# Kernel tuning notes

Measured on AMD Instinct MI355X. Metric: run time of the kernel, lower is better.

## Reference

```python
import jax, jax.numpy as jnp
import numpy as np
from jax import lax

DN = ('NHWC', 'HWIO', 'NHWC')

def hard_sigmoid(x):
    # Keras ConvLSTM2D default recurrent_activation
    return jnp.clip(0.2 * x + 0.5, 0.0, 1.0)

def conv2d_same(x, w):
    return lax.conv_general_dilated(x, w, (1, 1), 'SAME', dimension_numbers=DN)

def convlstm_layer(x, Wx, Wh, b):
    # x: [B,T,H,W,Cin]; Wx: [kh,kw,Cin,4F]; Wh: [kh,kw,F,4F]; b: [4F]
    B, T, H, W, Cin = x.shape
    F = Wh.shape[2]
    # Precompute input-to-gate convs for all timesteps in one big conv (same math).
    xg = conv2d_same(x.reshape(B * T, H, W, Cin), Wx).reshape(B, T, H, W, 4 * F) + b
    xg = jnp.moveaxis(xg, 1, 0)  # [T,B,H,W,4F]
    h0 = jnp.zeros((B, H, W, F), x.dtype)
    c0 = jnp.zeros((B, H, W, F), x.dtype)

    def step(carry, xg_t):
        h, c = carry
        gates = xg_t + conv2d_same(h, Wh)
        i, f, g, o = jnp.split(gates, 4, axis=-1)
        i = hard_sigmoid(i)
        f = hard_sigmoid(f)
        g = jnp.tanh(g)
        o = hard_sigmoid(o)
        c = f * c + i * g
        h = o * jnp.tanh(c)
        return (h, c), h

    (h, c), hs = lax.scan(step, (h0, c0), xg)
    outputs = jnp.moveaxis(hs, 0, 1)  # [B,T,H,W,F]
    return outputs, h, c

def setup_inputs() -> dict:
    key = jax.random.key(0)
    ks = jax.random.split(key, 8)
    B, T, H, W, Cin = 8, 10, 64, 64, 1
    F = 64
    k = 3
    sc = lambda fan: 1.0 / np.sqrt(fan)
    x = jax.random.normal(ks[0], (B, T, H, W, Cin), jnp.float32)
    Wx0 = jax.random.normal(ks[1], (k, k, Cin, 4 * F), jnp.float32) * sc(k * k * Cin)
    Wh0 = jax.random.normal(ks[2], (k, k, F, 4 * F), jnp.float32) * sc(k * k * F)
    b0 = jax.random.normal(ks[3], (4 * F,), jnp.float32) * 0.01
    Wx1 = jax.random.normal(ks[4], (k, k, F, 4 * F), jnp.float32) * sc(k * k * F)
    Wh1 = jax.random.normal(ks[5], (k, k, F, 4 * F), jnp.float32) * sc(k * k * F)
    b1 = jax.random.normal(ks[6], (4 * F,), jnp.float32) * 0.01
    return {'x': x, 'Wx0': Wx0, 'Wh0': Wh0, 'b0': b0, 'Wx1': Wx1, 'Wh1': Wh1, 'b1': b1}

def reference(x, Wx0, Wh0, b0, Wx1, Wh1, b1):
    out0, h0, c0 = convlstm_layer(x, Wx0, Wh0, b0)
    out1, h1, c1 = convlstm_layer(out0, Wx1, Wh1, b1)
    # Encoder returns per-layer [hidden_state, cell_state]; stack: [L,2,B,H,W,F]
    return jnp.stack([jnp.stack([h0, c0]), jnp.stack([h1, c1])])
```

## Files before the change

### kernel.cpp

```cpp
#include <hip/hip_runtime.h>


typedef _Float16 f16x8 __attribute__((ext_vector_type(8)));
typedef float f32x4 __attribute__((ext_vector_type(4)));

#define BHWF (8 * 64 * 64 * 64)
#define TSTRIDE 72
#define NCELL 180

__device__ __forceinline__ float hsig(float x) {
    return fminf(fmaxf(fmaf(0.2f, x, 0.5f), 0.0f), 1.0f);
}

__device__ __forceinline__ float ftanh(float x) {
    float e = __expf(2.0f * x);
    return fmaf(-2.0f, __builtin_amdgcn_rcpf(e + 1.0f), 1.0f);
}

__device__ __forceinline__ ushort f2h(float f) {
    _Float16 h = (_Float16)f;
    return __builtin_bit_cast(ushort, h);
}

__global__ void prep_w(const float* __restrict__ s0, const float* __restrict__ s1,
                       const float* __restrict__ s2, const float* __restrict__ wx0,
                       ushort* __restrict__ d0, ushort* __restrict__ d1,
                       ushort* __restrict__ d2, ushort* __restrict__ dx0) {
    int o = blockIdx.x * 256 + threadIdx.x;
    if (blockIdx.y == 3) {
        if (o < 8192) {
            int e    = o & 7;
            int lane = (o >> 3) & 63;
            int g    = (o >> 9) & 3;
            int fq   = (o >> 11) & 3;
            int k = (lane >> 4) * 8 + e;
            int n = g * 64 + fq * 16 + (lane & 15);
            dx0[o] = (k < 9) ? f2h(wx0[k * 256 + n]) : (ushort)0;
        }
        return;
    }
    const float* s[3] = { s0, s1, s2 };
    ushort* d[3] = { d0, d1, d2 };
    int e    = o & 7;
    int lane = (o >> 3) & 63;
    int g    = (o >> 9) & 3;
    int fq   = (o >> 11) & 3;
    int kc   = (o >> 13) & 1;
    int tap  = o >> 14;
    int n = g * 64 + fq * 16 + (lane & 15);
    int k = tap * 64 + kc * 32 + (lane >> 4) * 8 + e;
    d[blockIdx.y][o] = f2h(s[blockIdx.y][k * 256 + n]);
}

__device__ __forceinline__ void stage(const ushort* __restrict__ src,
                                      ushort* __restrict__ tile,
                                      int y0, int x0, int tid) {
    for (int v = tid; v < NCELL * 8; v += 256) {
        int cell = v >> 3, j = v & 7;
        int r = cell / 18, cc = cell - r * 18;
        int y = y0 - 1 + r, xx = x0 - 1 + cc;
        uint4 dv = make_uint4(0u, 0u, 0u, 0u);
        if ((unsigned)y < 64u && (unsigned)xx < 64u)
            dv = ((const uint4*)src)[(size_t)((y << 6) + xx) * 8 + j];
        *(uint4*)&tile[cell * TSTRIDE + j * 8] = dv;
    }
}

__device__ __forceinline__ void dma4(const ushort* __restrict__ src, ushort* dst) {
#pragma unroll
    for (int g = 0; g < 4; ++g)
        __builtin_amdgcn_global_load_lds(
            (const __attribute__((address_space(1))) unsigned int*)(src + g * 512),
            (__attribute__((address_space(3))) unsigned int*)(dst + g * 512),
            16, 0, 0);
}

__device__ __forceinline__ void conv_stream(const ushort* __restrict__ tile,
                                            const ushort* __restrict__ WS,
                                            ushort* __restrict__ bbuf,
                                            f32x4 (&acc)[8][4],
                                            int fq, int lane) {
    const int colA = lane & 15;
    const int quad = (lane >> 4) & 3;
    const int sl = fq * 2048 + lane * 8;
    dma4(WS + sl, bbuf + sl);
    f16x8 A[10];
#pragma unroll
    for (int c = 0; c < 18; ++c) {
        if (c < 17) {
            const int c1 = c + 1;
            const int kc1 = c1 / 9, dx1 = (c1 % 9) / 3, dy1 = c1 % 3;
            dma4(WS + (size_t)((dy1 * 3 + dx1) * 2 + kc1) * 8192 + sl,
                 bbuf + (c1 & 1) * 8192 + sl);
            __asm__ volatile("s_waitcnt vmcnt(4)" ::: "memory");
        } else {
            __asm__ volatile("s_waitcnt vmcnt(0)" ::: "memory");
        }
        const int kc = c / 9, dx = (c % 9) / 3, dy = c % 3;
        if (dy == 0) {
#pragma unroll
            for (int r = 0; r < 10; ++r)
                A[r] = *(const f16x8*)&tile[(r * 18 + colA + dx) * TSTRIDE + kc * 32 + quad * 8];
        }
        const ushort* bp = bbuf + (c & 1) * 8192 + sl;
        f16x8 B0 = *(const f16x8*)&bp[0];
        f16x8 B1 = *(const f16x8*)&bp[512];
        f16x8 B2 = *(const f16x8*)&bp[1024];
        f16x8 B3 = *(const f16x8*)&bp[1536];
#pragma unroll
        for (int mt = 0; mt < 8; ++mt) {
            acc[mt][0] = __builtin_amdgcn_mfma_f32_16x16x32_f16(A[mt + dy], B0, acc[mt][0], 0, 0, 0);
            acc[mt][1] = __builtin_amdgcn_mfma_f32_16x16x32_f16(A[mt + dy], B1, acc[mt][1], 0, 0, 0);
            acc[mt][2] = __builtin_amdgcn_mfma_f32_16x16x32_f16(A[mt + dy], B2, acc[mt][2], 0, 0, 0);
            acc[mt][3] = __builtin_amdgcn_mfma_f32_16x16x32_f16(A[mt + dy], B3, acc[mt][3], 0, 0, 0);
        }
    }
}

__global__ __launch_bounds__(256, 2) void step_merged(
    int l0_active, int l1_active, int last0, int last1,
    const float* __restrict__ x, const ushort* __restrict__ Wx0F,
    const ushort* __restrict__ Wh0S, const float* __restrict__ b0,
    const ushort* __restrict__ h0_prev, float* __restrict__ c0,
    ushort* __restrict__ h0_out, float* __restrict__ oh0, float* __restrict__ oc0,
    const ushort* __restrict__ xin, const ushort* __restrict__ Wx1S,
    const ushort* __restrict__ Wh1S, const float* __restrict__ b1,
    const ushort* __restrict__ h1_prev, float* __restrict__ c1,
    ushort* __restrict__ h1_out, float* __restrict__ oh1, float* __restrict__ oc1)
{
    __shared__ __align__(16) ushort tile[NCELL * TSTRIDE];
    __shared__ __align__(16) ushort bbuf[2 * 8192];
    __shared__ __align__(16) ushort xa[4096];

    const int z = blockIdx.z;
    bool isL1; int b;
    if (l0_active && l1_active) { isL1 = (z >= 8); b = z & 7; }
    else                        { isL1 = (l1_active != 0); b = z; }

    const int tid = threadIdx.x;
    const int lane = tid & 63;
    const int fq = tid >> 6;
    const int colA = lane & 15;
    const int quad = (lane >> 4) & 3;
    const int x0 = blockIdx.x * 16, y0 = blockIdx.y * 8;
    const int f = fq * 16 + colA;

    const ushort* h_prev = isL1 ? h1_prev : h0_prev;
    const float*  bias   = isL1 ? b1 : b0;
    float*        cbuf   = isL1 ? c1 : c0;
    ushort*       hout   = isL1 ? h1_out : h0_out;
    float* hf = isL1 ? (last1 ? oh1 : nullptr) : (last0 ? oh0 : nullptr);
    float* cf = isL1 ? (last1 ? oc1 : nullptr) : (last0 ? oc0 : nullptr);

    if (!isL1) {
        const float* xs = x + (size_t)b * 40960;
        for (int idx = tid; idx < 4096; idx += 256) {
            int e = idx & 7, li = (idx >> 3) & 63, r = idx >> 9;
            int ci = li & 15, qi = li >> 4;
            int k = qi * 8 + e;
            ushort val = 0;
            if (k < 9) {
                int dy = (k * 86) >> 8;
                int dx = k - dy * 3;
                int y = y0 + r + dy - 1, xx = x0 + ci + dx - 1;
                if ((unsigned)y < 64u && (unsigned)xx < 64u)
                    val = f2h(xs[(y << 6) + xx]);
            }
            xa[idx] = val;
        }
        if (h_prev) stage(h_prev + (size_t)b * 4096 * 64, tile, y0, x0, tid);
    } else {
        stage(xin + (size_t)b * 4096 * 64, tile, y0, x0, tid);
    }
    __syncthreads();

    f32x4 acc[8][4];
#pragma unroll
    for (int g = 0; g < 4; ++g) {
        float bv = bias[g * 64 + f];
#pragma unroll
        for (int mt = 0; mt < 8; ++mt) {
            acc[mt][g][0] = bv; acc[mt][g][1] = bv;
            acc[mt][g][2] = bv; acc[mt][g][3] = bv;
        }
    }

    if (!isL1) {
        f16x8 xb[4];
#pragma unroll
        for (int g = 0; g < 4; ++g)
            xb[g] = *(const f16x8*)&Wx0F[((fq * 4 + g) * 64 + lane) * 8];
#pragma unroll
        for (int mt = 0; mt < 8; ++mt) {
            f16x8 xaf = *(const f16x8*)&xa[mt * 512 + lane * 8];
#pragma unroll
            for (int g = 0; g < 4; ++g)
                acc[mt][g] = __builtin_amdgcn_mfma_f32_16x16x32_f16(
                    xaf, xb[g], acc[mt][g], 0, 0, 0);
        }
        if (h_prev) conv_stream(tile, Wh0S, bbuf, acc, fq, lane);
    } else {
        conv_stream(tile, Wx1S, bbuf, acc, fq, lane);
        if (h_prev) {
            __syncthreads();
            stage(h_prev + (size_t)b * 4096 * 64, tile, y0, x0, tid);
            __syncthreads();
            conv_stream(tile, Wh1S, bbuf, acc, fq, lane);
        }
    }

#pragma unroll
    for (int mt = 0; mt < 8; ++mt) {
        const int y = y0 + mt;
#pragma unroll
        for (int reg = 0; reg < 4; ++reg) {
            const int xx = x0 + quad * 4 + reg;
            const size_t cidx = ((size_t)((((b * 4 + fq) * 64 + y) * 4 + reg) * 16
                                 + (x0 >> 2) + quad)) * 16 + colA;
            const size_t pidx = ((size_t)b * 4096 + (y << 6) + xx) * 64 + f;
            float cp = h_prev ? cbuf[cidx] : 0.f;
            float iv = hsig(acc[mt][0][reg]);
            float fv = hsig(acc[mt][1][reg]);
            float gv = ftanh(acc[mt][2][reg]);
            float ov = hsig(acc[mt][3][reg]);
            float cn = fmaf(fv, cp, iv * gv);
            float hn = ov * ftanh(cn);
            cbuf[cidx] = cn;
            hout[pidx] = f2h(hn);
            if (hf) { hf[pidx] = hn; cf[pidx] = cn; }
        }
    }
}

extern "C" void kernel_launch(void* const* d_in, const int* in_sizes, int n_in,
                              void* d_out, int out_size, void* d_ws, size_t ws_size,
                              hipStream_t stream) {
    const float* x   = (const float*)d_in[0];
    const float* Wx0 = (const float*)d_in[1];
    const float* Wh0 = (const float*)d_in[2];
    const float* b0  = (const float*)d_in[3];
    const float* Wx1 = (const float*)d_in[4];
    const float* Wh1 = (const float*)d_in[5];
    const float* b1  = (const float*)d_in[6];
    float* out = (float*)d_out;
    char* ws = (char*)d_ws;

    ushort* h0buf[2] = { (ushort*)ws, (ushort*)(ws + 4u * 1024 * 1024) };
    ushort* h1buf[2] = { (ushort*)(ws + 8u * 1024 * 1024), (ushort*)(ws + 12u * 1024 * 1024) };
    float* c0 = (float*)(ws + 16u * 1024 * 1024);
    float* c1 = (float*)(ws + 24u * 1024 * 1024);
    ushort* Wh0S = (ushort*)(ws + 32u * 1024 * 1024);
    ushort* Wx1S = Wh0S + 147456;
    ushort* Wh1S = Wx1S + 147456;
    ushort* Wx0F = Wh1S + 147456;

    prep_w<<<dim3(576, 4), 256, 0, stream>>>(Wh0, Wx1, Wh1, Wx0,
                                             Wh0S, Wx1S, Wh1S, Wx0F);

    for (int t = 0; t <= 10; ++t) {
        const int has0 = (t < 10), has1 = (t >= 1);
        const int s = t - 1;
        const int tx = has0 ? t : 9;
        dim3 grid(4, 8, (has0 && has1) ? 16 : 8);
        step_merged<<<grid, 256, 0, stream>>>(
            has0, has1, (t == 9), (s == 9),
            x + (size_t)tx * 4096, Wx0F,
            (t >= 1) ? Wh0S : nullptr, b0,
            (t >= 1 && has0) ? h0buf[(t - 1) & 1] : nullptr, c0,
            h0buf[t & 1], out, out + BHWF,
            has1 ? h0buf[s & 1] : nullptr, Wx1S,
            Wh1S, b1,
            (s >= 1) ? h1buf[(s - 1) & 1] : nullptr, c1,
            h1buf[s & 1], out + 2 * (size_t)BHWF, out + 3 * (size_t)BHWF);
    }
}
```

Before: 461.0 us.

## Halve spatial tile height, load weights to registers, raise occupancy to four blocks

```diff
diff --git a/kernel.cpp b/kernel.cpp
--- a/kernel.cpp
+++ b/kernel.cpp
@@ -6,7 +6,7 @@
 
 #define BHWF (8 * 64 * 64 * 64)
 #define TSTRIDE 72
-#define NCELL 180
+#define NCELL 108
 
 __device__ __forceinline__ float hsig(float x) {
     return fminf(fmaxf(fmaf(0.2f, x, 0.5f), 0.0f), 1.0f);
@@ -66,58 +66,44 @@
     }
 }
 
-__device__ __forceinline__ void dma4(const ushort* __restrict__ src, ushort* dst) {
-#pragma unroll
-    for (int g = 0; g < 4; ++g)
-        __builtin_amdgcn_global_load_lds(
-            (const __attribute__((address_space(1))) unsigned int*)(src + g * 512),
-            (__attribute__((address_space(3))) unsigned int*)(dst + g * 512),
-            16, 0, 0);
-}
-
 __device__ __forceinline__ void conv_stream(const ushort* __restrict__ tile,
                                             const ushort* __restrict__ WS,
-                                            ushort* __restrict__ bbuf,
-                                            f32x4 (&acc)[8][4],
+                                            f32x4 (&acc)[4][4],
                                             int fq, int lane) {
     const int colA = lane & 15;
     const int quad = (lane >> 4) & 3;
-    const int sl = fq * 2048 + lane * 8;
-    dma4(WS + sl, bbuf + sl);
-    f16x8 A[10];
+    const ushort* wbase = WS + fq * 2048 + lane * 8;
+    f16x8 B[2][4];
+#pragma unroll
+    for (int g = 0; g < 4; ++g)
+        B[0][g] = *(const f16x8*)&wbase[g * 512];
 #pragma unroll
     for (int c = 0; c < 18; ++c) {
         if (c < 17) {
             const int c1 = c + 1;
             const int kc1 = c1 / 9, dx1 = (c1 % 9) / 3, dy1 = c1 % 3;
-            dma4(WS + (size_t)((dy1 * 3 + dx1) * 2 + kc1) * 8192 + sl,
-                 bbuf + (c1 & 1) * 8192 + sl);
-            __asm__ volatile("s_waitcnt vmcnt(4)" ::: "memory");
-        } else {
-            __asm__ volatile("s_waitcnt vmcnt(0)" ::: "memory");
+            const int f1 = (dy1 * 3 + dx1) * 2 + kc1;
+#pragma unroll
+            for (int g = 0; g < 4; ++g)
+                B[c1 & 1][g] = *(const f16x8*)&wbase[(size_t)f1 * 8192 + g * 512];
         }
         const int kc = c / 9, dx = (c % 9) / 3, dy = c % 3;
-        if (dy == 0) {
-#pragma unroll
-            for (int r = 0; r < 10; ++r)
-                A[r] = *(const f16x8*)&tile[(r * 18 + colA + dx) * TSTRIDE + kc * 32 + quad * 8];
-        }
-        const ushort* bp = bbuf + (c & 1) * 8192 + sl;
-        f16x8 B0 = *(const f16x8*)&bp[0];
-        f16x8 B1 = *(const f16x8*)&bp[512];
-        f16x8 B2 = *(const f16x8*)&bp[1024];
-        f16x8 B3 = *(const f16x8*)&bp[1536];
-#pragma unroll
-        for (int mt = 0; mt < 8; ++mt) {
-            acc[mt][0] = __builtin_amdgcn_mfma_f32_16x16x32_f16(A[mt + dy], B0, acc[mt][0], 0, 0, 0);
-            acc[mt][1] = __builtin_amdgcn_mfma_f32_16x16x32_f16(A[mt + dy], B1, acc[mt][1], 0, 0, 0);
-            acc[mt][2] = __builtin_amdgcn_mfma_f32_16x16x32_f16(A[mt + dy], B2, acc[mt][2], 0, 0, 0);
-            acc[mt][3] = __builtin_amdgcn_mfma_f32_16x16x32_f16(A[mt + dy], B3, acc[mt][3], 0, 0, 0);
-        }
-    }
-}
-
-__global__ __launch_bounds__(256, 2) void step_merged(
+        const ushort* ap = &tile[(dy * 18 + colA + dx) * TSTRIDE + kc * 32 + quad * 8];
+        f16x8 a0 = *(const f16x8*)&ap[0 * 18 * TSTRIDE];
+        f16x8 a1 = *(const f16x8*)&ap[1 * 18 * TSTRIDE];
+        f16x8 a2 = *(const f16x8*)&ap[2 * 18 * TSTRIDE];
+        f16x8 a3 = *(const f16x8*)&ap[3 * 18 * TSTRIDE];
+#pragma unroll
+        for (int g = 0; g < 4; ++g) {
+            acc[0][g] = __builtin_amdgcn_mfma_f32_16x16x32_f16(a0, B[c & 1][g], acc[0][g], 0, 0, 0);
+            acc[1][g] = __builtin_amdgcn_mfma_f32_16x16x32_f16(a1, B[c & 1][g], acc[1][g], 0, 0, 0);
+            acc[2][g] = __builtin_amdgcn_mfma_f32_16x16x32_f16(a2, B[c & 1][g], acc[2][g], 0, 0, 0);
+            acc[3][g] = __builtin_amdgcn_mfma_f32_16x16x32_f16(a3, B[c & 1][g], acc[3][g], 0, 0, 0);
+        }
+    }
+}
+
+__global__ __launch_bounds__(256, 4) void step_merged(
     int l0_active, int l1_active, int last0, int last1,
     const float* __restrict__ x, const ushort* __restrict__ Wx0F,
     const ushort* __restrict__ Wh0S, const float* __restrict__ b0,
@@ -129,8 +115,7 @@
     ushort* __restrict__ h1_out, float* __restrict__ oh1, float* __restrict__ oc1)
 {
     __shared__ __align__(16) ushort tile[NCELL * TSTRIDE];
-    __shared__ __align__(16) ushort bbuf[2 * 8192];
-    __shared__ __align__(16) ushort xa[4096];
+    __shared__ __align__(16) ushort xa[2048];
 
     const int z = blockIdx.z;
     bool isL1; int b;
@@ -142,7 +127,7 @@
     const int fq = tid >> 6;
     const int colA = lane & 15;
     const int quad = (lane >> 4) & 3;
-    const int x0 = blockIdx.x * 16, y0 = blockIdx.y * 8;
+    const int x0 = blockIdx.x * 16, y0 = blockIdx.y * 4;
     const int f = fq * 16 + colA;
 
     const ushort* h_prev = isL1 ? h1_prev : h0_prev;
@@ -154,7 +139,7 @@
 
     if (!isL1) {
         const float* xs = x + (size_t)b * 40960;
-        for (int idx = tid; idx < 4096; idx += 256) {
+        for (int idx = tid; idx < 2048; idx += 256) {
             int e = idx & 7, li = (idx >> 3) & 63, r = idx >> 9;
             int ci = li & 15, qi = li >> 4;
             int k = qi * 8 + e;
@@ -174,12 +159,12 @@
     }
     __syncthreads();
 
-    f32x4 acc[8][4];
+    f32x4 acc[4][4];
 #pragma unroll
     for (int g = 0; g < 4; ++g) {
         float bv = bias[g * 64 + f];
 #pragma unroll
-        for (int mt = 0; mt < 8; ++mt) {
+        for (int mt = 0; mt < 4; ++mt) {
             acc[mt][g][0] = bv; acc[mt][g][1] = bv;
             acc[mt][g][2] = bv; acc[mt][g][3] = bv;
         }
@@ -191,26 +176,26 @@
         for (int g = 0; g < 4; ++g)
             xb[g] = *(const f16x8*)&Wx0F[((fq * 4 + g) * 64 + lane) * 8];
 #pragma unroll
-        for (int mt = 0; mt < 8; ++mt) {
+        for (int mt = 0; mt < 4; ++mt) {
             f16x8 xaf = *(const f16x8*)&xa[mt * 512 + lane * 8];
 #pragma unroll
             for (int g = 0; g < 4; ++g)
                 acc[mt][g] = __builtin_amdgcn_mfma_f32_16x16x32_f16(
                     xaf, xb[g], acc[mt][g], 0, 0, 0);
         }
-        if (h_prev) conv_stream(tile, Wh0S, bbuf, acc, fq, lane);
+        if (h_prev) conv_stream(tile, Wh0S, acc, fq, lane);
     } else {
-        conv_stream(tile, Wx1S, bbuf, acc, fq, lane);
+        conv_stream(tile, Wx1S, acc, fq, lane);
         if (h_prev) {
             __syncthreads();
             stage(h_prev + (size_t)b * 4096 * 64, tile, y0, x0, tid);
             __syncthreads();
-            conv_stream(tile, Wh1S, bbuf, acc, fq, lane);
-        }
-    }
-
-#pragma unroll
-    for (int mt = 0; mt < 8; ++mt) {
+            conv_stream(tile, Wh1S, acc, fq, lane);
+        }
+    }
+
+#pragma unroll
+    for (int mt = 0; mt < 4; ++mt) {
         const int y = y0 + mt;
 #pragma unroll
         for (int reg = 0; reg < 4; ++reg) {
@@ -261,7 +246,7 @@
         const int has0 = (t < 10), has1 = (t >= 1);
         const int s = t - 1;
         const int tx = has0 ? t : 9;
-        dim3 grid(4, 8, (has0 && has1) ? 16 : 8);
+        dim3 grid(4, 16, (has0 && has1) ? 16 : 8);
         step_merged<<<grid, 256, 0, stream>>>(
             has0, has1, (t == 9), (s == 9),
             x + (size_t)tx * 4096, Wx0F,
```

New measurement: 586.6 us. 1.27x slower.

## Share weight frames across block with triple-buffered cooperative DMA and barriers

Applied to the files above, without the earlier changes.

```diff
diff --git a/kernel.cpp b/kernel.cpp
--- a/kernel.cpp
+++ b/kernel.cpp
@@ -66,12 +66,18 @@
     }
 }
 
-__device__ __forceinline__ void dma4(const ushort* __restrict__ src, ushort* dst) {
-#pragma unroll
-    for (int g = 0; g < 4; ++g)
+__device__ __forceinline__ int frame_of(int c) {
+    int kc = c / 9, r = c % 9, dxx = r / 3, dyy = r % 3;
+    return (dyy * 3 + dxx) * 2 + kc;
+}
+
+__device__ __forceinline__ void dma_frame(const ushort* __restrict__ src,
+                                          ushort* __restrict__ dst, int tid) {
+#pragma unroll
+    for (int s = 0; s < 4; ++s)
         __builtin_amdgcn_global_load_lds(
-            (const __attribute__((address_space(1))) unsigned int*)(src + g * 512),
-            (__attribute__((address_space(3))) unsigned int*)(dst + g * 512),
+            (const __attribute__((address_space(1))) unsigned int*)(src + s * 2048 + tid * 8),
+            (__attribute__((address_space(3))) unsigned int*)(dst + s * 2048 + tid * 8),
             16, 0, 0);
 }
 
@@ -79,30 +85,27 @@
                                             const ushort* __restrict__ WS,
                                             ushort* __restrict__ bbuf,
                                             f32x4 (&acc)[8][4],
-                                            int fq, int lane) {
+                                            int fq, int lane, int tid) {
     const int colA = lane & 15;
     const int quad = (lane >> 4) & 3;
-    const int sl = fq * 2048 + lane * 8;
-    dma4(WS + sl, bbuf + sl);
+    __syncthreads();
+    dma_frame(WS + (size_t)frame_of(0) * 8192, bbuf, tid);
+    dma_frame(WS + (size_t)frame_of(1) * 8192, bbuf + 8192, tid);
+    __asm__ volatile("s_waitcnt vmcnt(4)\ns_barrier" ::: "memory");
     f16x8 A[10];
 #pragma unroll
     for (int c = 0; c < 18; ++c) {
-        if (c < 17) {
-            const int c1 = c + 1;
-            const int kc1 = c1 / 9, dx1 = (c1 % 9) / 3, dy1 = c1 % 3;
-            dma4(WS + (size_t)((dy1 * 3 + dx1) * 2 + kc1) * 8192 + sl,
-                 bbuf + (c1 & 1) * 8192 + sl);
-            __asm__ volatile("s_waitcnt vmcnt(4)" ::: "memory");
-        } else {
-            __asm__ volatile("s_waitcnt vmcnt(0)" ::: "memory");
-        }
+        if (c <= 15)
+            dma_frame(WS + (size_t)frame_of(c + 2) * 8192,
+                      bbuf + ((c + 2) % 3) * 8192, tid);
         const int kc = c / 9, dx = (c % 9) / 3, dy = c % 3;
         if (dy == 0) {
 #pragma unroll
             for (int r = 0; r < 10; ++r)
-                A[r] = *(const f16x8*)&tile[(r * 18 + colA + dx) * TSTRIDE + kc * 32 + quad * 8];
-        }
-        const ushort* bp = bbuf + (c & 1) * 8192 + sl;
+                A[r] = *(const f16x8*)&tile[(r * 18 + colA + dx) * TSTRIDE
+                                            + kc * 32 + quad * 8];
+        }
+        const ushort* bp = bbuf + (c % 3) * 8192 + fq * 2048 + lane * 8;
         f16x8 B0 = *(const f16x8*)&bp[0];
         f16x8 B1 = *(const f16x8*)&bp[512];
         f16x8 B2 = *(const f16x8*)&bp[1024];
@@ -114,6 +117,12 @@
             acc[mt][2] = __builtin_amdgcn_mfma_f32_16x16x32_f16(A[mt + dy], B2, acc[mt][2], 0, 0, 0);
             acc[mt][3] = __builtin_amdgcn_mfma_f32_16x16x32_f16(A[mt + dy], B3, acc[mt][3], 0, 0, 0);
         }
+        if (c <= 15)
+            __asm__ volatile("s_waitcnt vmcnt(4)\ns_barrier" ::: "memory");
+        else if (c == 16)
+            __asm__ volatile("s_waitcnt vmcnt(0)\ns_barrier" ::: "memory");
+        else
+            __asm__ volatile("s_barrier" ::: "memory");
     }
 }
 
@@ -129,8 +138,8 @@
     ushort* __restrict__ h1_out, float* __restrict__ oh1, float* __restrict__ oc1)
 {
     __shared__ __align__(16) ushort tile[NCELL * TSTRIDE];
-    __shared__ __align__(16) ushort bbuf[2 * 8192];
-    __shared__ __align__(16) ushort xa[4096];
+    __shared__ __align__(16) ushort bbuf[3 * 8192];
+    ushort* xa = bbuf;
 
     const int z = blockIdx.z;
     bool isL1; int b;
@@ -143,6 +152,7 @@
     const int colA = lane & 15;
     const int quad = (lane >> 4) & 3;
     const int x0 = blockIdx.x * 16, y0 = blockIdx.y * 8;
+    const int blk = blockIdx.y * 4 + blockIdx.x;
     const int f = fq * 16 + colA;
 
     const ushort* h_prev = isL1 ? h1_prev : h0_prev;
@@ -198,14 +208,14 @@
                 acc[mt][g] = __builtin_amdgcn_mfma_f32_16x16x32_f16(
                     xaf, xb[g], acc[mt][g], 0, 0, 0);
         }
-        if (h_prev) conv_stream(tile, Wh0S, bbuf, acc, fq, lane);
+        if (h_prev) conv_stream(tile, Wh0S, bbuf, acc, fq, lane, tid);
     } else {
-        conv_stream(tile, Wx1S, bbuf, acc, fq, lane);
+        conv_stream(tile, Wx1S, bbuf, acc, fq, lane, tid);
         if (h_prev) {
             __syncthreads();
             stage(h_prev + (size_t)b * 4096 * 64, tile, y0, x0, tid);
             __syncthreads();
-            conv_stream(tile, Wh1S, bbuf, acc, fq, lane);
+            conv_stream(tile, Wh1S, bbuf, acc, fq, lane, tid);
         }
     }
 
@@ -215,8 +225,8 @@
 #pragma unroll
         for (int reg = 0; reg < 4; ++reg) {
             const int xx = x0 + quad * 4 + reg;
-            const size_t cidx = ((size_t)((((b * 4 + fq) * 64 + y) * 4 + reg) * 16
-                                 + (x0 >> 2) + quad)) * 16 + colA;
+            const size_t cidx = (((((size_t)b * 32 + blk) * 4 + fq) * 8 + mt) * 4
+                                 + reg) * 64 + lane;
             const size_t pidx = ((size_t)b * 4096 + (y << 6) + xx) * 64 + f;
             float cp = h_prev ? cbuf[cidx] : 0.f;
             float iv = hsig(acc[mt][0][reg]);
```

Measured after the change: 469.2 us. No clear change (+1.8%).
